# Performance work log

Hardware: AMD Instinct MI355X
Metric: run time of the kernel (lower is better)

The kernel has to match this reference:

```python
import jax, jax.numpy as jnp
import numpy as np

B, XDIM, TWIN, INCH = 1024, 62, 10, 128
MID, OUT, K, K1, LIN, HC = 256, 512, 3, 10, 512, 4
EPS = 1e-5

REGIONS = [
    list(range(0, 5)),
    list(range(5, 8)) + list(range(14, 17)),
    list(range(8, 11)) + list(range(17, 20)),
    list(range(11, 14)) + list(range(20, 23)),
    list(range(23, 26)) + list(range(32, 35)),
    list(range(26, 29)) + list(range(35, 38)),
    list(range(29, 32)) + list(range(38, 41)),
    list(range(41, 44)) + list(range(50, 52)) + list(range(57, 58)),
    list(range(44, 47)) + list(range(52, 55)) + list(range(58, 61)),
    list(range(47, 50)) + list(range(55, 57)) + list(range(61, 62)),
]


def setup_inputs() -> dict:
    key = jax.random.key(0)
    ks = jax.random.split(key, 40)
    n = lambda k, s, sc=0.02: jax.random.normal(k, s, jnp.float32) * sc
    inp = {
        "x": jax.random.normal(ks[0], (B, XDIM, TWIN, INCH), jnp.float32),
        "tfe_w": n(ks[1], (XDIM, TWIN)),          # depthwise Conv2d (10,1) weight, squeezed
        "tfe_b": jnp.zeros((XDIM,), jnp.float32),
        "cheby1_w": n(ks[2], (K, INCH, OUT)),
        "A": n(ks[3], (XDIM, XDIM)),
        "cheby2_w": n(ks[4], (K, MID, OUT)),
        "A1": n(ks[5], (K1, K1)),
        "b_gate": jnp.float32(1.0),
        "c_gate": jnp.float32(1.0),
        "region_b": jnp.zeros((K1, MID), jnp.float32),
        "hc_w1": n(ks[6], (OUT * 72, LIN)),
        "hc_b1": jnp.zeros((LIN,), jnp.float32),
        "bn1_g": jnp.ones((LIN,), jnp.float32),
        "bn1_b": jnp.zeros((LIN,), jnp.float32),
        "hc_w2": n(ks[7], (LIN, LIN // 2)),
        "hc_b2": jnp.zeros((LIN // 2,), jnp.float32),
        "bn2_g": jnp.ones((LIN // 2,), jnp.float32),
        "bn2_b": jnp.zeros((LIN // 2,), jnp.float32),
        "hc_w3": n(ks[8], (LIN // 2, HC)),
        "hc_b3": jnp.zeros((HC,), jnp.float32),
    }
    for i, idx in enumerate(REGIONS):
        inp[f"rw{i+1}"] = n(ks[10 + i], (MID, INCH, len(idx)))
    return inp


def _cheby(x, L, Ws):
    # sum_k  S_k @ x @ W_k  with S_0 = I, S_k = S_{k-1} @ L ; then ReLU
    S = jnp.eye(L.shape[0], dtype=x.dtype)
    res = jnp.zeros(x.shape[:2] + (Ws.shape[-1],), x.dtype)
    for k in range(Ws.shape[0]):
        res = res + jnp.einsum("nm,bmt,to->bno", S, x, Ws[k])
        S = S @ L
    return jax.nn.relu(res)


def _bn(h, g, b):
    mu = h.mean(axis=0)
    v = h.var(axis=0)  # biased, training-mode BatchNorm1d
    return (h - mu) * jax.lax.rsqrt(v + EPS) * g + b


def _forward(x, tfe_w, tfe_b, cheby1_w, A, cheby2_w, A1, b_gate, c_gate,
             rw1, rw2, rw3, rw4, rw5, rw6, rw7, rw8, rw9, rw10, region_b,
             hc_w1, hc_b1, bn1_g, bn1_b, hc_w2, hc_b2, bn2_g, bn2_b, hc_w3, hc_b3):
    # variance gate (torch.var default: unbiased)
    sigma = jnp.var(x, axis=2, ddof=1)                              # (B, 62, INCH)
    g_tfe = jnp.einsum("bcit,ci->bct", x, tfe_w) + tfe_b[None, :, None]
    g = g_tfe * jnp.exp(-sigma)                                      # (B, 62, INCH)

    g1 = _cheby(g, A, cheby1_w)                                      # (B, 62, OUT)

    rws = [rw1, rw2, rw3, rw4, rw5, rw6, rw7, rw8, rw9, rw10]
    RG = []
    for i, (idx, w) in enumerate(zip(REGIONS, rws)):
        reg = g[:, jnp.asarray(idx), :]                              # (B, L, INCH)
        RG.append(jnp.einsum("blc,mcl->bm", reg, w) + region_b[i])   # Conv1d, full-width kernel
    g2in = jnp.stack(RG, axis=1)                                     # (B, 10, MID)
    g2 = _cheby(g2in, A1, cheby2_w)                                  # (B, 10, OUT)

    att = jnp.concatenate([b_gate * g1, c_gate * g2], axis=1)        # (B, 72, OUT)
    cat = jnp.concatenate([g1, g2], axis=1)
    out = jax.nn.softmax(att, axis=1) * cat
    out = out.reshape(out.shape[0], -1)                              # (B, 72*OUT)

    h = jax.nn.gelu(_bn(out @ hc_w1 + hc_b1, bn1_g, bn1_b), approximate=False)
    h = jax.nn.gelu(_bn(h @ hc_w2 + hc_b2, bn2_g, bn2_b), approximate=False)
    h = h @ hc_w3 + hc_b3
    return jax.nn.softmax(h, axis=1)


def reference(x, tfe_w, tfe_b, cheby1_w, A, cheby2_w, A1, b_gate, c_gate,
              rw1, rw2, rw3, rw4, rw5, rw6, rw7, rw8, rw9, rw10, region_b,
              hc_w1, hc_b1, bn1_g, bn1_b, hc_w2, hc_b2, bn2_g, bn2_b, hc_w3, hc_b3):
    return _forward(x, tfe_w, tfe_b, cheby1_w, A, cheby2_w, A1, b_gate, c_gate,
                    rw1, rw2, rw3, rw4, rw5, rw6, rw7, rw8, rw9, rw10, region_b,
                    hc_w1, hc_b1, bn1_g, bn1_b, hc_w2, hc_b2, bn2_g, bn2_b, hc_w3, hc_b3)
```

## Files before the change

kernel.cpp:

```cpp
#include <hip/hip_runtime.h>
#include <math.h>


__constant__ int cOrder[62] = {
  0,1,2,3,4,
  5,6,7,14,15,16,
  8,9,10,17,18,19,
  11,12,13,20,21,22,
  23,24,25,32,33,34,
  26,27,28,35,36,37,
  29,30,31,38,39,40,
  41,42,43,50,51,57,
  44,45,46,52,53,54,58,59,60,
  47,48,49,55,56,61
};
__constant__ int cPos[62] = {
  0,1,2,3,4, 5,6,7, 11,12,13, 17,18,19, 8,9,10, 14,15,16, 20,21,22,
  23,24,25, 29,30,31, 35,36,37, 26,27,28, 32,33,34, 38,39,40,
  41,42,43, 47,48,49, 56,57,58, 44,45, 50,51,52, 59,60, 46, 53,54,55, 61
};
__constant__ int cRegK[10]   = {640,768,768,768,768,768,768,768,1152,768};
__constant__ int cRegCum[10] = {0,640,1408,2176,2944,3712,4480,5248,6016,7168};

struct Ptr10 { const float* p[10]; };

typedef __attribute__((ext_vector_type(8))) short bf16x8;
typedef __attribute__((ext_vector_type(4))) float f32x4;

__device__ __forceinline__ float gelu_exact(float v){
  return 0.5f * v * (1.0f + erff(v * 0.70710678118654752f));
}
__device__ __forceinline__ unsigned short f2bf(float f){
  unsigned u = __float_as_uint(f);
  unsigned r = (u + 0x7fffu + ((u >> 16) & 1u)) >> 16;
  return (unsigned short)r;
}
__device__ __forceinline__ float bf2f(unsigned short u){
  return __uint_as_float(((unsigned)u) << 16);
}
__device__ __forceinline__ void load_lds16(const unsigned short* g, unsigned short* l){
  __builtin_amdgcn_global_load_lds(
      (const __attribute__((address_space(1))) void*)g,
      (__attribute__((address_space(3))) void*)l, 16, 0, 0);
}

template<bool RELU>
__global__ __launch_bounds__(256) void k_mfma(
    const unsigned short* __restrict__ A, long lda,
    const unsigned short* __restrict__ BT, long ldb,
    void* __restrict__ Cv, int ldc, int kPerZ, long cStrideZ){
  __shared__ unsigned short As[128*32];
  __shared__ unsigned short Bs[128*32];
  int tid = threadIdx.x;
  int wave = tid >> 6, lane = tid & 63;
  int m0 = blockIdx.x * 128, n0 = blockIdx.y * 128;
  int kStart = blockIdx.z * kPerZ;
  int waveM = wave >> 1, waveN = wave & 1;
  int lr = lane >> 2, ch = lane & 3;
  int quad = lane >> 4, mrow = lane & 15;
  int swe = ((quad ^ (mrow & 3)) << 3);

  int rA0 = wave*32 + lr;
  int rA1 = rA0 + 16;
  int ce  = ((ch ^ (rA0 & 3)) << 3);
  const unsigned short* gA0 = A  + (long)(m0 + rA0)*lda + kStart + ce;
  const unsigned short* gA1 = A  + (long)(m0 + rA1)*lda + kStart + ce;
  const unsigned short* gB0 = BT + (long)(n0 + rA0)*ldb + kStart + ce;
  const unsigned short* gB1 = BT + (long)(n0 + rA1)*ldb + kStart + ce;
  unsigned short* lA0 = &As[(wave*32)*32];
  unsigned short* lA1 = &As[(wave*32+16)*32];
  unsigned short* lB0 = &Bs[(wave*32)*32];
  unsigned short* lB1 = &Bs[(wave*32+16)*32];

  f32x4 acc[4][4] = {};
  int nIter = kPerZ >> 5;
  for (int it = 0; it < nIter; ++it){
    long ko = (long)it << 5;
    load_lds16(gA0 + ko, lA0);
    load_lds16(gA1 + ko, lA1);
    load_lds16(gB0 + ko, lB0);
    load_lds16(gB1 + ko, lB1);
    __syncthreads();
    bf16x8 af[4], bfr[4];
#pragma unroll
    for (int mi = 0; mi < 4; mi++)
      af[mi] = *(const bf16x8*)&As[(waveM*64 + mi*16 + mrow)*32 + swe];
#pragma unroll
    for (int ni = 0; ni < 4; ni++)
      bfr[ni] = *(const bf16x8*)&Bs[(waveN*64 + ni*16 + mrow)*32 + swe];
#pragma unroll
    for (int mi = 0; mi < 4; mi++)
#pragma unroll
      for (int ni = 0; ni < 4; ni++)
        acc[mi][ni] = __builtin_amdgcn_mfma_f32_16x16x32_bf16(
            af[mi], bfr[ni], acc[mi][ni], 0, 0, 0);
    __syncthreads();
  }
  if (RELU){
    unsigned short* C = (unsigned short*)Cv;
#pragma unroll
    for (int mi = 0; mi < 4; mi++)
#pragma unroll
      for (int ni = 0; ni < 4; ni++){
        int col = n0 + waveN*64 + ni*16 + mrow;
#pragma unroll
        for (int r = 0; r < 4; r++){
          int row = m0 + waveM*64 + mi*16 + quad*4 + r;
          C[(long)row*ldc + col] = f2bf(fmaxf(acc[mi][ni][r], 0.f));
        }
      }
  } else {
    float* C = (float*)Cv + (long)blockIdx.z * cStrideZ;
#pragma unroll
    for (int mi = 0; mi < 4; mi++)
#pragma unroll
      for (int ni = 0; ni < 4; ni++){
        int col = n0 + waveN*64 + ni*16 + mrow;
#pragma unroll
        for (int r = 0; r < 4; r++){
          int row = m0 + waveM*64 + mi*16 + quad*4 + r;
          C[(long)row*ldc + col] = acc[mi][ni][r];
        }
      }
  }
}
template __global__ void k_mfma<true>(const unsigned short*, long, const unsigned short*, long, void*, int, int, long);
template __global__ void k_mfma<false>(const unsigned short*, long, const unsigned short*, long, void*, int, int, long);

__global__ __launch_bounds__(256) void k_mfma_region(
    const unsigned short* __restrict__ ARb,
    const unsigned short* __restrict__ RWT,
    const float* __restrict__ regb, float* __restrict__ g2in){
  __shared__ unsigned short As[128*32];
  __shared__ unsigned short Bs[128*32];
  int z = blockIdx.z;
  int K = cRegK[z];
  int cumk = cRegCum[z];
  const unsigned short* A  = ARb + cumk;
  const unsigned short* BT = RWT + (long)cumk*256;
  long lda = 7936, ldb = K;
  int tid = threadIdx.x;
  int wave = tid >> 6, lane = tid & 63;
  int m0 = blockIdx.x * 128, n0 = blockIdx.y * 128;
  int waveM = wave >> 1, waveN = wave & 1;
  int lr = lane >> 2, ch = lane & 3;
  int quad = lane >> 4, mrow = lane & 15;
  int swe = ((quad ^ (mrow & 3)) << 3);

  int rA0 = wave*32 + lr;
  int rA1 = rA0 + 16;
  int ce  = ((ch ^ (rA0 & 3)) << 3);
  const unsigned short* gA0 = A  + (long)(m0 + rA0)*lda + ce;
  const unsigned short* gA1 = A  + (long)(m0 + rA1)*lda + ce;
  const unsigned short* gB0 = BT + (long)(n0 + rA0)*ldb + ce;
  const unsigned short* gB1 = BT + (long)(n0 + rA1)*ldb + ce;
  unsigned short* lA0 = &As[(wave*32)*32];
  unsigned short* lA1 = &As[(wave*32+16)*32];
  unsigned short* lB0 = &Bs[(wave*32)*32];
  unsigned short* lB1 = &Bs[(wave*32+16)*32];

  f32x4 acc[4][4] = {};
  int nIter = K >> 5;
  for (int it = 0; it < nIter; ++it){
    long ko = (long)it << 5;
    load_lds16(gA0 + ko, lA0);
    load_lds16(gA1 + ko, lA1);
    load_lds16(gB0 + ko, lB0);
    load_lds16(gB1 + ko, lB1);
    __syncthreads();
    bf16x8 af[4], bfr[4];
#pragma unroll
    for (int mi = 0; mi < 4; mi++)
      af[mi] = *(const bf16x8*)&As[(waveM*64 + mi*16 + mrow)*32 + swe];
#pragma unroll
    for (int ni = 0; ni < 4; ni++)
      bfr[ni] = *(const bf16x8*)&Bs[(waveN*64 + ni*16 + mrow)*32 + swe];
#pragma unroll
    for (int mi = 0; mi < 4; mi++)
#pragma unroll
      for (int ni = 0; ni < 4; ni++)
        acc[mi][ni] = __builtin_amdgcn_mfma_f32_16x16x32_bf16(
            af[mi], bfr[ni], acc[mi][ni], 0, 0, 0);
    __syncthreads();
  }
#pragma unroll
  for (int mi = 0; mi < 4; mi++)
#pragma unroll
    for (int ni = 0; ni < 4; ni++){
      int col = n0 + waveN*64 + ni*16 + mrow;
      float bias = regb[z*256 + col];
#pragma unroll
      for (int r = 0; r < 4; r++){
        int row = m0 + waveM*64 + mi*16 + quad*4 + r;
        g2in[(long)row*2560 + z*256 + col] = acc[mi][ni][r] + bias;
      }
    }
}

__global__ __launch_bounds__(256) void k_prep_t(
    const float* __restrict__ s0, unsigned short* __restrict__ d0,
    const float* __restrict__ s1, unsigned short* __restrict__ d1,
    const float* __restrict__ s2, unsigned short* __restrict__ d2,
    const float* __restrict__ s3, unsigned short* __restrict__ d3){
  __shared__ float t[64][65];
  int id = blockIdx.x;
  const float* src; unsigned short* dst; int R, C, rt, ct;
  if (id < 4608){ src=s0; dst=d0; R=36864; C=512; rt=id>>3;  ct=id&7; }
  else if (id < 4640){ int q=id-4608; src=s1; dst=d1; R=512; C=256; rt=q>>2; ct=q&3; }
  else if (id < 4688){ int q=id-4640; src=s2; dst=d2; R=384; C=512; rt=q>>3; ct=q&7; }
  else { int q=id-4688; src=s3; dst=d3; R=768; C=512; rt=q>>3; ct=q&7; }
  int r0 = rt*64, c0 = ct*64;
  int tid = threadIdx.x;
  int rr = tid >> 2, cb = (tid & 3) << 2;
#pragma unroll
  for (int i = 0; i < 4; i++){
    int cc = cb + i*16;
    float4 v = *(const float4*)(src + (long)(r0+rr)*C + c0 + cc);
    t[rr][cc+0]=v.x; t[rr][cc+1]=v.y; t[rr][cc+2]=v.z; t[rr][cc+3]=v.w;
  }
  __syncthreads();
  int cc = tid >> 2, rb = (tid & 3) << 2;
#pragma unroll
  for (int i = 0; i < 4; i++){
    int r = rb + i*16;
    ushort4 u = make_ushort4(f2bf(t[r+0][cc]), f2bf(t[r+1][cc]),
                             f2bf(t[r+2][cc]), f2bf(t[r+3][cc]));
    *(ushort4*)(dst + (long)(c0+cc)*R + r0 + r) = u;
  }
}

__global__ __launch_bounds__(128) void k_rwt(Ptr10 rws, unsigned short* __restrict__ RWT){
  __shared__ float sld[1152];
  int z = blockIdx.y, m = blockIdx.x;
  int K = cRegK[z], L = K >> 7;
  const float* rw = rws.p[z] + (long)m*K;
  unsigned short* dst = RWT + (long)cRegCum[z]*256 + (long)m*K;
  for (int i = threadIdx.x; i < K; i += 128) sld[i] = rw[i];
  __syncthreads();
  for (int k = threadIdx.x; k < K; k += 128){
    int l = k >> 7, c = k & 127;
    dst[k] = f2bf(sld[c*L + l]);
  }
}

__global__ __launch_bounds__(64) void k_a2(
    const float* __restrict__ A, float* __restrict__ AT, float* __restrict__ A2T){
  __shared__ float arow[62];
  int r = blockIdx.x, c = threadIdx.x;
  if (c < 62) arow[c] = A[r*62 + c];
  __syncthreads();
  if (c < 62){
    AT[c*62 + r] = arow[c];
    float s = 0.f;
    for (int t = 0; t < 62; t++) s = fmaf(arow[t], A[t*62 + c], s);
    A2T[c*62 + r] = s;
  }
}

__global__ __launch_bounds__(128) void k_g(
    const float* __restrict__ x, const float* __restrict__ tw,
    const float* __restrict__ tb, unsigned short* __restrict__ arb,
    unsigned short* __restrict__ xcat){
  int bid = blockIdx.x;
  int b = bid / 62, n = bid - b*62;
  int t = threadIdx.x;
  const float* xp = x + (long)bid * 1280 + t;
  float s = 0.f, s2 = 0.f, gv = 0.f;
#pragma unroll
  for (int i = 0; i < 10; i++){
    float v = xp[(long)i*128];
    s += v; s2 = fmaf(v, v, s2);
    gv = fmaf(v, tw[n*10 + i], gv);
  }
  float mean = s * 0.1f;
  float var  = (s2 - 10.f*mean*mean) * (1.f/9.f);
  float res  = (gv + tb[n]) * expf(-var);
  unsigned short rb = f2bf(res);
  arb[(long)b*7936 + cPos[n]*128 + t] = rb;
  xcat[(long)b*23808 + n*384 + t]     = rb;
}

__global__ __launch_bounds__(256) void k_spread2(
    const unsigned short* __restrict__ ARb, const float* __restrict__ AT,
    const float* __restrict__ A2T, unsigned short* __restrict__ xcat){
  __shared__ float sgn[7936];
  int b = blockIdx.x, tid = threadIdx.x;
  for (int i = tid; i < 7936; i += 256){
    int p = i >> 7, c = i & 127;
    sgn[cOrder[p]*128 + c] = bf2f(ARb[(long)b*7936 + i]);
  }
  __syncthreads();
  int c = tid & 127, mat = tid >> 7;
  const float* MT = mat ? A2T : AT;
  float acc[62];
#pragma unroll
  for (int n = 0; n < 62; n++) acc[n] = 0.f;
  for (int m = 0; m < 62; m++){
    float gv = sgn[m*128 + c];
    const float* Mp = MT + m*62;
#pragma unroll
    for (int n = 0; n < 62; n++) acc[n] = fmaf(Mp[n], gv, acc[n]);
  }
  long base = (long)b*23808 + (mat+1)*128 + c;
#pragma unroll
  for (int n = 0; n < 62; n++) xcat[base + (long)n*384] = f2bf(acc[n]);
}

__global__ __launch_bounds__(256) void k_x2cat(
    const float* __restrict__ g2in, const float* __restrict__ A1,
    unsigned short* __restrict__ X2){
  __shared__ float sg[2560];
  __shared__ float sA1[100];
  __shared__ float sA2[100];
  int b = blockIdx.x, tid = threadIdx.x;
  for (int i = tid; i < 2560; i += 256) sg[i] = g2in[(long)b*2560 + i];
  if (tid < 100) sA1[tid] = A1[tid];
  __syncthreads();
  if (tid < 100){
    int n = tid/10, m = tid - n*10;
    float a = 0.f;
#pragma unroll
    for (int t = 0; t < 10; t++) a = fmaf(sA1[n*10+t], sA1[t*10+m], a);
    sA2[tid] = a;
  }
  __syncthreads();
  for (int i = tid; i < 2560; i += 256){
    int n = i >> 8, t = i & 255;
    float v1 = 0.f, v2 = 0.f;
#pragma unroll
    for (int m = 0; m < 10; m++){
      float gv = sg[(m<<8) + t];
      v1 = fmaf(sA1[n*10+m], gv, v1);
      v2 = fmaf(sA2[n*10+m], gv, v2);
    }
    long base = (long)b*7680 + n*768;
    X2[base + t]       = f2bf(sg[i]);
    X2[base + 256 + t] = f2bf(v1);
    X2[base + 512 + t] = f2bf(v2);
  }
}

__global__ __launch_bounds__(128) void k_softcat(
    const unsigned short* __restrict__ g1, const unsigned short* __restrict__ g2,
    const float* __restrict__ bg_, const float* __restrict__ cg_,
    unsigned short* __restrict__ outb){
  __shared__ float sc[72][128];
  int b = blockIdx.x;
  int oq = blockIdx.y * 128;
  int tid = threadIdx.x;
  int o = oq + tid;
#pragma unroll
  for (int j = 0; j < 62; j++) sc[j][tid] = bf2f(g1[((long)b*62 + j)*512 + o]);
#pragma unroll
  for (int j = 0; j < 10; j++) sc[62+j][tid] = bf2f(g2[((long)b*10 + j)*512 + o]);
  __syncthreads();
  float bg = *bg_, cg = *cg_;
  float mx = -1e30f;
#pragma unroll
  for (int j = 0; j < 72; j++){
    float av = (j < 62 ? bg : cg) * sc[j][tid];
    mx = fmaxf(mx, av);
  }
  float sum = 0.f;
#pragma unroll
  for (int j = 0; j < 72; j++){
    float av = (j < 62 ? bg : cg) * sc[j][tid];
    sum += expf(av - mx);
  }
  float inv = 1.f / sum;
#pragma unroll
  for (int j = 0; j < 72; j++){
    float v = sc[j][tid];
    float av = (j < 62 ? bg : cg) * v;
    outb[(long)b*36864 + j*512 + o] = f2bf(expf(av - mx) * inv * v);
  }
}

__global__ __launch_bounds__(256) void k_reduce(
    const float* __restrict__ P, float* __restrict__ h1){
  int idx = blockIdx.x*256 + threadIdx.x;
  float v = 0.f;
#pragma unroll
  for (int s = 0; s < 16; s++) v += P[(long)s*524288 + idx];
  h1[idx] = v;
}

template<int N>
__global__ __launch_bounds__(256) void k_stats(
    const float* __restrict__ h, float* __restrict__ mu, float* __restrict__ rs){
  __shared__ float ls[256], ls2[256];
  int j0 = blockIdx.x * 8;
  int jj = threadIdx.x & 7, bg = threadIdx.x >> 3;
  float s = 0.f, s2 = 0.f;
#pragma unroll 4
  for (int it = 0; it < 32; it++){
    float v = h[(long)(it*32 + bg)*N + j0 + jj];
    s += v; s2 = fmaf(v, v, s2);
  }
  ls[threadIdx.x] = s; ls2[threadIdx.x] = s2;
  __syncthreads();
  if (threadIdx.x < 8){
    float a = ls[threadIdx.x], a2 = ls2[threadIdx.x];
    for (int g = 1; g < 32; g++){ a += ls[g*8 + threadIdx.x]; a2 += ls2[g*8 + threadIdx.x]; }
    float m = a * (1.f/1024.f);
    float var = a2 * (1.f/1024.f) - m*m;
    mu[j0 + threadIdx.x] = m;
    rs[j0 + threadIdx.x] = rsqrtf(var + 1e-5f);
  }
}

__global__ __launch_bounds__(256) void k_bngelu(
    const float* __restrict__ h1, const float* __restrict__ mu,
    const float* __restrict__ rs, const float* __restrict__ gam,
    const float* __restrict__ bet, unsigned short* __restrict__ h1b){
  int base = (blockIdx.x*256 + threadIdx.x) * 4;
  int j = base & 511;
  float4 v = *(const float4*)(h1 + base);
  ushort4 u;
  u.x = f2bf(gelu_exact((v.x - mu[j+0])*rs[j+0]*gam[j+0] + bet[j+0]));
  u.y = f2bf(gelu_exact((v.y - mu[j+1])*rs[j+1]*gam[j+1] + bet[j+1]));
  u.z = f2bf(gelu_exact((v.z - mu[j+2])*rs[j+2]*gam[j+2] + bet[j+2]));
  u.w = f2bf(gelu_exact((v.w - mu[j+3])*rs[j+3]*gam[j+3] + bet[j+3]));
  *(ushort4*)(h1b + base) = u;
}

__global__ __launch_bounds__(256) void k_final(
    const float* __restrict__ h2, const float* __restrict__ mu,
    const float* __restrict__ rs, const float* __restrict__ gam,
    const float* __restrict__ bet, const float* __restrict__ w3,
    const float* __restrict__ b3, float* __restrict__ outp){
  int b = blockIdx.x, tid = threadIdx.x;
  float v = h2[(long)b*256 + tid];
  v = (v - mu[tid]) * rs[tid] * gam[tid] + bet[tid];
  v = gelu_exact(v);
  float4 w = ((const float4*)w3)[tid];
  float p0 = v*w.x, p1 = v*w.y, p2 = v*w.z, p3 = v*w.w;
#pragma unroll
  for (int o = 32; o > 0; o >>= 1){
    p0 += __shfl_down(p0, o);
    p1 += __shfl_down(p1, o);
    p2 += __shfl_down(p2, o);
    p3 += __shfl_down(p3, o);
  }
  __shared__ float red[4][4];
  int wv = tid >> 6;
  if ((tid & 63) == 0){ red[wv][0]=p0; red[wv][1]=p1; red[wv][2]=p2; red[wv][3]=p3; }
  __syncthreads();
  if (tid == 0){
    float l[4];
#pragma unroll
    for (int c = 0; c < 4; c++)
      l[c] = red[0][c]+red[1][c]+red[2][c]+red[3][c] + b3[c];
    float m = fmaxf(fmaxf(l[0], l[1]), fmaxf(l[2], l[3]));
    float e[4]; float sum = 0.f;
#pragma unroll
    for (int c = 0; c < 4; c++){ e[c] = expf(l[c]-m); sum += e[c]; }
    float inv = 1.f / sum;
#pragma unroll
    for (int c = 0; c < 4; c++) outp[(long)b*4 + c] = e[c]*inv;
  }
}

extern "C" void kernel_launch(void* const* d_in, const int* in_sizes, int n_in,
                              void* d_out, int out_size, void* d_ws, size_t ws_size,
                              hipStream_t stream){
  (void)n_in; (void)out_size; (void)ws_size;
  bool dictOrder = (in_sizes[9] == 2560);
  const float* x     = (const float*)d_in[0];
  const float* tfe_w = (const float*)d_in[1];
  const float* tfe_b = (const float*)d_in[2];
  const float* ch1w  = (const float*)d_in[3];
  const float* Amat  = (const float*)d_in[4];
  const float* ch2w  = (const float*)d_in[5];
  const float* A1mat = (const float*)d_in[6];
  const float* bgate = (const float*)d_in[7];
  const float* cgate = (const float*)d_in[8];
  const float* regb  = (const float*)d_in[dictOrder ? 9 : 19];
  int o = dictOrder ? 0 : 10;
  const float* hc_w1 = (const float*)d_in[10+o];
  const float* bn1g  = (const float*)d_in[12+o];
  const float* bn1b  = (const float*)d_in[13+o];
  const float* hc_w2 = (const float*)d_in[14+o];
  const float* bn2g  = (const float*)d_in[16+o];
  const float* bn2b  = (const float*)d_in[17+o];
  const float* hc_w3 = (const float*)d_in[18+o];
  const float* hc_b3 = (const float*)d_in[19+o];
  Ptr10 rws;
  for (int i = 0; i < 10; i++) rws.p[i] = (const float*)d_in[(dictOrder ? 20 : 9) + i];

  char* Wb = (char*)d_ws;
  unsigned short* ARb   = (unsigned short*)(Wb + 0);
  unsigned short* XCAT  = (unsigned short*)(Wb + 16252928);
  unsigned short* RWT   = (unsigned short*)(Wb + 65011712);
  float*          G2IN  = (float*)(Wb + 69074944);
  unsigned short* X2CAT = (unsigned short*)(Wb + 79560704);
  unsigned short* W1T   = (unsigned short*)(Wb + 95289344);
  unsigned short* WC1T  = (unsigned short*)(Wb + 133038080);
  unsigned short* WC2T  = (unsigned short*)(Wb + 133431296);
  unsigned short* G1    = (unsigned short*)(Wb + 134217728);
  unsigned short* G2    = (unsigned short*)(Wb + 199229440);
  unsigned short* OUTB  = (unsigned short*)(Wb + 0);
  float*          P     = (float*)(Wb + 209715200);
  float*          H1    = (float*)(Wb + 243269632);
  float*          H2    = (float*)(Wb + 245366784);
  float*          MU1   = (float*)(Wb + 246415360);
  float*          RS1   = MU1 + 512;
  float*          MU2   = MU1 + 1024;
  float*          RS2   = MU1 + 1280;
  float*          AT    = (float*)(Wb + 246423552);
  float*          A2T   = (float*)(Wb + 246439040);
  unsigned short* W2T   = (unsigned short*)(Wb + 246454528);
  unsigned short* H1B   = (unsigned short*)(Wb + 246716928);

  k_prep_t<<<4784, 256, 0, stream>>>(hc_w1, W1T, hc_w2, W2T, ch1w, WC1T, ch2w, WC2T);
  k_rwt<<<dim3(256,10), 128, 0, stream>>>(rws, RWT);
  k_a2<<<62, 64, 0, stream>>>(Amat, AT, A2T);

  k_g<<<1024*62, 128, 0, stream>>>(x, tfe_w, tfe_b, ARb, XCAT);
  k_spread2<<<1024, 256, 0, stream>>>(ARb, AT, A2T, XCAT);
  k_mfma_region<<<dim3(8,2,10), 256, 0, stream>>>(ARb, RWT, regb, G2IN);
  k_x2cat<<<1024, 256, 0, stream>>>(G2IN, A1mat, X2CAT);
  k_mfma<true><<<dim3(80,4,1), 256, 0, stream>>>(X2CAT, 768, WC2T, 768, (void*)G2, 512, 768, 0);
  k_mfma<true><<<dim3(496,4,1), 256, 0, stream>>>(XCAT, 384, WC1T, 384, (void*)G1, 512, 384, 0);
  k_softcat<<<dim3(1024,4), 128, 0, stream>>>(G1, G2, bgate, cgate, OUTB);
  k_mfma<false><<<dim3(8,4,16), 256, 0, stream>>>(OUTB, 36864, W1T, 36864, (void*)P, 512, 2304, 524288);
  k_reduce<<<2048, 256, 0, stream>>>(P, H1);
  k_stats<512><<<64, 256, 0, stream>>>(H1, MU1, RS1);
  k_bngelu<<<512, 256, 0, stream>>>(H1, MU1, RS1, bn1g, bn1b, H1B);
  k_mfma<false><<<dim3(8,2,1), 256, 0, stream>>>(H1B, 512, W2T, 512, (void*)H2, 256, 512, 0);
  k_stats<256><<<32, 256, 0, stream>>>(H2, MU2, RS2);
  k_final<<<1024, 256, 0, stream>>>(H2, MU2, RS2, bn2g, bn2b, hc_w3, hc_b3, (float*)d_out);
}
```

Before: 948.1 us.

## Fuse prep kernels, merge gating with spread, remap GEMM blocks for XCD locality

Merges the three weight-prep kernels into one launch, and fuses the per-node gating kernel with the graph spread kernel so the gated features stay in LDS instead of being round-tripped through global bf16. GEMM launches switch to a 1D grid with a block-id remapping that puts groups of 8 neighbouring tiles (sharing A rows) on the same XCD, aiming at better L2 reuse. The softmax-gating kernel caches exp*v in LDS to avoid recomputing expf, and the split-K reduction uses float4 loads. The fused gspread kernel runs a 31-iteration serial loop per block, which may lower parallelism compared with the old 63K-block gating launch.

```diff
diff --git a/kernel.cpp b/kernel.cpp
--- a/kernel.cpp
+++ b/kernel.cpp
@@ -48,13 +48,23 @@
 __global__ __launch_bounds__(256) void k_mfma(
     const unsigned short* __restrict__ A, long lda,
     const unsigned short* __restrict__ BT, long ldb,
-    void* __restrict__ Cv, int ldc, int kPerZ, long cStrideZ){
+    void* __restrict__ Cv, int ldc, int kPerZ, long cStrideZ, int mcCount){
   __shared__ unsigned short As[128*32];
   __shared__ unsigned short Bs[128*32];
+  int mt, nt, zt;
+  if (mcCount){
+    int id = blockIdx.x;
+    int c = ((id >> 6) << 3) + (id & 7);
+    int member = (id >> 3) & 7;
+    zt = c / mcCount;
+    int mc = c - zt*mcCount;
+    mt = mc*2 + (member >> 2);
+    nt = member & 3;
+  } else { mt = blockIdx.x; nt = blockIdx.y; zt = blockIdx.z; }
   int tid = threadIdx.x;
   int wave = tid >> 6, lane = tid & 63;
-  int m0 = blockIdx.x * 128, n0 = blockIdx.y * 128;
-  int kStart = blockIdx.z * kPerZ;
+  int m0 = mt * 128, n0 = nt * 128;
+  int kStart = zt * kPerZ;
   int waveM = wave >> 1, waveN = wave & 1;
   int lr = lane >> 2, ch = lane & 3;
   int quad = lane >> 4, mrow = lane & 15;
@@ -110,7 +120,7 @@
         }
       }
   } else {
-    float* C = (float*)Cv + (long)blockIdx.z * cStrideZ;
+    float* C = (float*)Cv + (long)zt * cStrideZ;
 #pragma unroll
     for (int mi = 0; mi < 4; mi++)
 #pragma unroll
@@ -124,8 +134,8 @@
       }
   }
 }
-template __global__ void k_mfma<true>(const unsigned short*, long, const unsigned short*, long, void*, int, int, long);
-template __global__ void k_mfma<false>(const unsigned short*, long, const unsigned short*, long, void*, int, int, long);
+template __global__ void k_mfma<true>(const unsigned short*, long, const unsigned short*, long, void*, int, int, long, int);
+template __global__ void k_mfma<false>(const unsigned short*, long, const unsigned short*, long, void*, int, int, long, int);
 
 __global__ __launch_bounds__(256) void k_mfma_region(
     const unsigned short* __restrict__ ARb,
@@ -197,101 +207,97 @@
     }
 }
 
-__global__ __launch_bounds__(256) void k_prep_t(
+__global__ __launch_bounds__(256) void k_prep_all(
     const float* __restrict__ s0, unsigned short* __restrict__ d0,
     const float* __restrict__ s1, unsigned short* __restrict__ d1,
     const float* __restrict__ s2, unsigned short* __restrict__ d2,
-    const float* __restrict__ s3, unsigned short* __restrict__ d3){
-  __shared__ float t[64][65];
+    const float* __restrict__ s3, unsigned short* __restrict__ d3,
+    Ptr10 rws, unsigned short* __restrict__ RWT,
+    const float* __restrict__ Amat, float* __restrict__ AT,
+    float* __restrict__ A2T){
+  __shared__ float smem[64*65];
   int id = blockIdx.x;
+  int tid = threadIdx.x;
+  if (id < 7344 && id >= 4784){
+    int q = id - 4784;
+    int z = q >> 8, m = q & 255;
+    int K = cRegK[z], L = K >> 7;
+    const float* rw = rws.p[z] + (long)m*K;
+    unsigned short* dst = RWT + (long)cRegCum[z]*256 + (long)m*K;
+    for (int i = tid; i < K; i += 256) smem[i] = rw[i];
+    __syncthreads();
+    for (int k = tid; k < K; k += 256){
+      int l = k >> 7, c = k & 127;
+      dst[k] = f2bf(smem[c*L + l]);
+    }
+    return;
+  }
+  if (id >= 7344){
+    int r = id - 7344, c = tid;
+    if (c < 62) smem[c] = Amat[r*62 + c];
+    __syncthreads();
+    if (c < 62){
+      AT[c*62 + r] = smem[c];
+      float s = 0.f;
+      for (int t = 0; t < 62; t++) s = fmaf(smem[t], Amat[t*62 + c], s);
+      A2T[c*62 + r] = s;
+    }
+    return;
+  }
   const float* src; unsigned short* dst; int R, C, rt, ct;
   if (id < 4608){ src=s0; dst=d0; R=36864; C=512; rt=id>>3;  ct=id&7; }
   else if (id < 4640){ int q=id-4608; src=s1; dst=d1; R=512; C=256; rt=q>>2; ct=q&3; }
   else if (id < 4688){ int q=id-4640; src=s2; dst=d2; R=384; C=512; rt=q>>3; ct=q&7; }
   else { int q=id-4688; src=s3; dst=d3; R=768; C=512; rt=q>>3; ct=q&7; }
   int r0 = rt*64, c0 = ct*64;
-  int tid = threadIdx.x;
   int rr = tid >> 2, cb = (tid & 3) << 2;
 #pragma unroll
   for (int i = 0; i < 4; i++){
     int cc = cb + i*16;
     float4 v = *(const float4*)(src + (long)(r0+rr)*C + c0 + cc);
-    t[rr][cc+0]=v.x; t[rr][cc+1]=v.y; t[rr][cc+2]=v.z; t[rr][cc+3]=v.w;
+    smem[rr*65+cc+0]=v.x; smem[rr*65+cc+1]=v.y;
+    smem[rr*65+cc+2]=v.z; smem[rr*65+cc+3]=v.w;
   }
   __syncthreads();
   int cc = tid >> 2, rb = (tid & 3) << 2;
 #pragma unroll
   for (int i = 0; i < 4; i++){
     int r = rb + i*16;
-    ushort4 u = make_ushort4(f2bf(t[r+0][cc]), f2bf(t[r+1][cc]),
-                             f2bf(t[r+2][cc]), f2bf(t[r+3][cc]));
+    ushort4 u = make_ushort4(f2bf(smem[(r+0)*65+cc]), f2bf(smem[(r+1)*65+cc]),
+                             f2bf(smem[(r+2)*65+cc]), f2bf(smem[(r+3)*65+cc]));
     *(ushort4*)(dst + (long)(c0+cc)*R + r0 + r) = u;
   }
 }
 
-__global__ __launch_bounds__(128) void k_rwt(Ptr10 rws, unsigned short* __restrict__ RWT){
-  __shared__ float sld[1152];
-  int z = blockIdx.y, m = blockIdx.x;
-  int K = cRegK[z], L = K >> 7;
-  const float* rw = rws.p[z] + (long)m*K;
-  unsigned short* dst = RWT + (long)cRegCum[z]*256 + (long)m*K;
-  for (int i = threadIdx.x; i < K; i += 128) sld[i] = rw[i];
-  __syncthreads();
-  for (int k = threadIdx.x; k < K; k += 128){
-    int l = k >> 7, c = k & 127;
-    dst[k] = f2bf(sld[c*L + l]);
-  }
-}
-
-__global__ __launch_bounds__(64) void k_a2(
-    const float* __restrict__ A, float* __restrict__ AT, float* __restrict__ A2T){
-  __shared__ float arow[62];
-  int r = blockIdx.x, c = threadIdx.x;
-  if (c < 62) arow[c] = A[r*62 + c];
-  __syncthreads();
-  if (c < 62){
-    AT[c*62 + r] = arow[c];
-    float s = 0.f;
-    for (int t = 0; t < 62; t++) s = fmaf(arow[t], A[t*62 + c], s);
-    A2T[c*62 + r] = s;
-  }
-}
-
-__global__ __launch_bounds__(128) void k_g(
+__global__ __launch_bounds__(256) void k_gspread(
     const float* __restrict__ x, const float* __restrict__ tw,
-    const float* __restrict__ tb, unsigned short* __restrict__ arb,
+    const float* __restrict__ tb, const float* __restrict__ AT,
+    const float* __restrict__ A2T, unsigned short* __restrict__ arb,
     unsigned short* __restrict__ xcat){
-  int bid = blockIdx.x;
-  int b = bid / 62, n = bid - b*62;
-  int t = threadIdx.x;
-  const float* xp = x + (long)bid * 1280 + t;
-  float s = 0.f, s2 = 0.f, gv = 0.f;
-#pragma unroll
-  for (int i = 0; i < 10; i++){
-    float v = xp[(long)i*128];
-    s += v; s2 = fmaf(v, v, s2);
-    gv = fmaf(v, tw[n*10 + i], gv);
-  }
-  float mean = s * 0.1f;
-  float var  = (s2 - 10.f*mean*mean) * (1.f/9.f);
-  float res  = (gv + tb[n]) * expf(-var);
-  unsigned short rb = f2bf(res);
-  arb[(long)b*7936 + cPos[n]*128 + t] = rb;
-  xcat[(long)b*23808 + n*384 + t]     = rb;
-}
-
-__global__ __launch_bounds__(256) void k_spread2(
-    const unsigned short* __restrict__ ARb, const float* __restrict__ AT,
-    const float* __restrict__ A2T, unsigned short* __restrict__ xcat){
   __shared__ float sgn[7936];
   int b = blockIdx.x, tid = threadIdx.x;
-  for (int i = tid; i < 7936; i += 256){
-    int p = i >> 7, c = i & 127;
-    sgn[cOrder[p]*128 + c] = bf2f(ARb[(long)b*7936 + i]);
-  }
-  __syncthreads();
-  int c = tid & 127, mat = tid >> 7;
-  const float* MT = mat ? A2T : AT;
+  int c = tid & 127, half = tid >> 7;
+  const float* xb = x + (long)b * 79360;
+  for (int nn = 0; nn < 31; nn++){
+    int n = nn*2 + half;
+    const float* xp = xb + (long)n*1280 + c;
+    float s = 0.f, s2 = 0.f, gv = 0.f;
+#pragma unroll
+    for (int i = 0; i < 10; i++){
+      float v = xp[i*128];
+      s += v; s2 = fmaf(v, v, s2);
+      gv = fmaf(v, tw[n*10 + i], gv);
+    }
+    float mean = s * 0.1f;
+    float var  = (s2 - 10.f*mean*mean) * (1.f/9.f);
+    float res  = (gv + tb[n]) * expf(-var);
+    sgn[n*128 + c] = res;
+    unsigned short rb = f2bf(res);
+    arb[(long)b*7936 + cPos[n]*128 + c] = rb;
+    xcat[(long)b*23808 + n*384 + c]     = rb;
+  }
+  __syncthreads();
+  const float* MT = half ? A2T : AT;
   float acc[62];
 #pragma unroll
   for (int n = 0; n < 62; n++) acc[n] = 0.f;
@@ -301,7 +307,7 @@
 #pragma unroll
     for (int n = 0; n < 62; n++) acc[n] = fmaf(Mp[n], gv, acc[n]);
   }
-  long base = (long)b*23808 + (mat+1)*128 + c;
+  long base = (long)b*23808 + (half+1)*128 + c;
 #pragma unroll
   for (int n = 0; n < 62; n++) xcat[base + (long)n*384] = f2bf(acc[n]);
 }
@@ -364,24 +370,26 @@
   float sum = 0.f;
 #pragma unroll
   for (int j = 0; j < 72; j++){
-    float av = (j < 62 ? bg : cg) * sc[j][tid];
-    sum += expf(av - mx);
+    float v = sc[j][tid];
+    float e = expf((j < 62 ? bg : cg) * v - mx);
+    sum += e;
+    sc[j][tid] = e * v;
   }
   float inv = 1.f / sum;
 #pragma unroll
-  for (int j = 0; j < 72; j++){
-    float v = sc[j][tid];
-    float av = (j < 62 ? bg : cg) * v;
-    outb[(long)b*36864 + j*512 + o] = f2bf(expf(av - mx) * inv * v);
-  }
+  for (int j = 0; j < 72; j++)
+    outb[(long)b*36864 + j*512 + o] = f2bf(sc[j][tid] * inv);
 }
 
 __global__ __launch_bounds__(256) void k_reduce(
-    const float* __restrict__ P, float* __restrict__ h1){
+    const float4* __restrict__ P, float4* __restrict__ h1){
   int idx = blockIdx.x*256 + threadIdx.x;
-  float v = 0.f;
-#pragma unroll
-  for (int s = 0; s < 16; s++) v += P[(long)s*524288 + idx];
+  float4 v = make_float4(0.f,0.f,0.f,0.f);
+#pragma unroll
+  for (int s = 0; s < 16; s++){
+    float4 p = P[(long)s*131072 + idx];
+    v.x += p.x; v.y += p.y; v.z += p.z; v.w += p.w;
+  }
   h1[idx] = v;
 }
 
@@ -512,22 +520,19 @@
   unsigned short* W2T   = (unsigned short*)(Wb + 246454528);
   unsigned short* H1B   = (unsigned short*)(Wb + 246716928);
 
-  k_prep_t<<<4784, 256, 0, stream>>>(hc_w1, W1T, hc_w2, W2T, ch1w, WC1T, ch2w, WC2T);
-  k_rwt<<<dim3(256,10), 128, 0, stream>>>(rws, RWT);
-  k_a2<<<62, 64, 0, stream>>>(Amat, AT, A2T);
-
-  k_g<<<1024*62, 128, 0, stream>>>(x, tfe_w, tfe_b, ARb, XCAT);
-  k_spread2<<<1024, 256, 0, stream>>>(ARb, AT, A2T, XCAT);
+  k_prep_all<<<7406, 256, 0, stream>>>(hc_w1, W1T, hc_w2, W2T, ch1w, WC1T,
+                                       ch2w, WC2T, rws, RWT, Amat, AT, A2T);
+  k_gspread<<<1024, 256, 0, stream>>>(x, tfe_w, tfe_b, AT, A2T, ARb, XCAT);
   k_mfma_region<<<dim3(8,2,10), 256, 0, stream>>>(ARb, RWT, regb, G2IN);
   k_x2cat<<<1024, 256, 0, stream>>>(G2IN, A1mat, X2CAT);
-  k_mfma<true><<<dim3(80,4,1), 256, 0, stream>>>(X2CAT, 768, WC2T, 768, (void*)G2, 512, 768, 0);
-  k_mfma<true><<<dim3(496,4,1), 256, 0, stream>>>(XCAT, 384, WC1T, 384, (void*)G1, 512, 384, 0);
+  k_mfma<true><<<320, 256, 0, stream>>>(X2CAT, 768, WC2T, 768, (void*)G2, 512, 768, 0, 40);
+  k_mfma<true><<<1984, 256, 0, stream>>>(XCAT, 384, WC1T, 384, (void*)G1, 512, 384, 0, 248);
   k_softcat<<<dim3(1024,4), 128, 0, stream>>>(G1, G2, bgate, cgate, OUTB);
-  k_mfma<false><<<dim3(8,4,16), 256, 0, stream>>>(OUTB, 36864, W1T, 36864, (void*)P, 512, 2304, 524288);
-  k_reduce<<<2048, 256, 0, stream>>>(P, H1);
+  k_mfma<false><<<512, 256, 0, stream>>>(OUTB, 36864, W1T, 36864, (void*)P, 512, 2304, 524288, 4);
+  k_reduce<<<512, 256, 0, stream>>>((const float4*)P, (float4*)H1);
   k_stats<512><<<64, 256, 0, stream>>>(H1, MU1, RS1);
   k_bngelu<<<512, 256, 0, stream>>>(H1, MU1, RS1, bn1g, bn1b, H1B);
-  k_mfma<false><<<dim3(8,2,1), 256, 0, stream>>>(H1B, 512, W2T, 512, (void*)H2, 256, 512, 0);
+  k_mfma<false><<<dim3(8,2,1), 256, 0, stream>>>(H1B, 512, W2T, 512, (void*)H2, 256, 512, 0, 0);
   k_stats<256><<<32, 256, 0, stream>>>(H2, MU2, RS2);
   k_final<<<1024, 256, 0, stream>>>(H2, MU2, RS2, bn2g, bn2b, hc_w3, hc_b3, (float*)d_out);
 }
```

Measured after the change: 952.3 us. No clear change (+0.4%).
